# Kernel optimization log

Measured on AMD Instinct MI355X. Metric: run time of the kernel, lower is better.

The kernel has to match this reference:

```python
import jax, jax.numpy as jnp
import numpy as np

B, S, D = 2, 2048, 1024
H, DK = 16, 64
NUM_BUCKETS, MAX_DIST = 32, 128
EPS = 1e-6


def _relative_position_bucket(q_len, k_len):
    # T5 bidirectional relative position bucketing.
    ctx = jnp.arange(q_len)[:, None]
    mem = jnp.arange(k_len)[None, :]
    rel = mem - ctx  # [q, k]
    nb = NUM_BUCKETS // 2
    ret = (rel > 0).astype(jnp.int32) * nb
    n = jnp.abs(rel)
    max_exact = nb // 2
    is_small = n < max_exact
    n_safe = jnp.maximum(n, 1).astype(jnp.float32)
    val_large = max_exact + (
        jnp.log(n_safe / max_exact) / np.log(MAX_DIST / max_exact) * (nb - max_exact)
    ).astype(jnp.int32)
    val_large = jnp.minimum(val_large, nb - 1)
    return ret + jnp.where(is_small, n, val_large)  # [q, k] int32


def setup_inputs() -> dict:
    key = jax.random.key(0)
    ks = jax.random.split(key, 7)
    s = 0.02
    return {
        "hidden_states": jax.random.normal(ks[0], (B, S, D), jnp.float32),
        "ln_g": jnp.ones((D,), jnp.float32),
        "ln_b": jnp.zeros((D,), jnp.float32),
        "Wq": jax.random.normal(ks[1], (D, H * DK), jnp.float32) * s,
        "Wk": jax.random.normal(ks[2], (D, H * DK), jnp.float32) * s,
        "Wv": jax.random.normal(ks[3], (D, H * DK), jnp.float32) * s,
        "Wo": jax.random.normal(ks[4], (H * DK, D), jnp.float32) * s,
        "rel_bias": jax.random.normal(ks[5], (NUM_BUCKETS, H), jnp.float32) * s,
    }


def reference(hidden_states, ln_g, ln_b, Wq, Wk, Wv, Wo, rel_bias):
    b, s, d = hidden_states.shape
    # LayerNorm (nn.LayerNorm with affine, biased variance)
    mu = jnp.mean(hidden_states, axis=-1, keepdims=True)
    var = jnp.mean(jnp.square(hidden_states - mu), axis=-1, keepdims=True)
    normed = (hidden_states - mu) * jax.lax.rsqrt(var + EPS) * ln_g + ln_b
    # QKV projections (no bias), split heads
    q = (normed @ Wq).reshape(b, s, H, DK)
    k = (normed @ Wk).reshape(b, s, H, DK)
    v = (normed @ Wv).reshape(b, s, H, DK)
    # T5 attention: NO 1/sqrt(d) scaling; learned relative-position bias added to logits
    scores = jnp.einsum("bqhd,bkhd->bhqk", q, k)
    bucket = _relative_position_bucket(s, s)          # [s, s]
    bias = jnp.transpose(rel_bias[bucket], (2, 0, 1))  # [H, s, s]
    attn = jax.nn.softmax(scores + bias[None], axis=-1)
    ctx = jnp.einsum("bhqk,bkhd->bqhd", attn, v).reshape(b, s, H * DK)
    out = ctx @ Wo
    # residual (dropout is identity in eval)
    return hidden_states + out
```

## Files before the change

kernel.cpp:

```cpp
#include <hip/hip_runtime.h>
#include <hip/hip_bf16.h>
#include <math.h>

typedef __attribute__((__ext_vector_type__(8))) short bf16x8;
typedef __attribute__((__ext_vector_type__(4))) float f32x4;
typedef __attribute__((__ext_vector_type__(16))) float f32x16;
typedef __attribute__((__ext_vector_type__(4))) unsigned int u32x4;

#define B_ 2
#define S_ 2048
#define D_ 1024
#define H_ 16
#define DK_ 64
#define M_ (B_*S_)
#define N3_ 3072
#define BIAS_LEN 4096
#define M0_ 24.0f
#define L2E_ 1.4426950408889634f

__device__ __forceinline__ unsigned short f2bf(float f){
  union { float f; unsigned int u; } v; v.f = f;
  unsigned int u = v.u;
  unsigned int r = (u + 0x7fffu + ((u >> 16) & 1u)) >> 16;
  return (unsigned short)r;
}

__device__ __forceinline__ unsigned int pkbf(float a, float b){
  return ((unsigned int)f2bf(b) << 16) | (unsigned int)f2bf(a);
}

__device__ __forceinline__ float fexp2(float x){
#if __has_builtin(__builtin_amdgcn_exp2f)
  return __builtin_amdgcn_exp2f(x);
#else
  return __expf(x * 0.6931471805599453f);
#endif
}

__device__ __forceinline__ f32x4 zero4(){
  f32x4 z; z[0]=0.f; z[1]=0.f; z[2]=0.f; z[3]=0.f; return z;
}

__device__ __forceinline__ f32x4 mfma16(bf16x8 a, bf16x8 b, f32x4 c){
  return __builtin_amdgcn_mfma_f32_16x16x32_bf16(a, b, c, 0, 0, 0);
}
__device__ __forceinline__ f32x16 mfma32(bf16x8 a, bf16x8 b, f32x16 c){
  return __builtin_amdgcn_mfma_f32_32x32x16_bf16(a, b, c, 0, 0, 0);
}

__global__ __launch_bounds__(256) void transpose_cast_kernel(
    const float* __restrict__ Wq, const float* __restrict__ Wk,
    const float* __restrict__ Wv, const float* __restrict__ Wo,
    unsigned short* __restrict__ Wcat_t, unsigned short* __restrict__ Wo_t)
{
  __shared__ float tile[64][65];
  const int k0 = blockIdx.x * 64;
  const int v0 = blockIdx.y * 64;
  const int sel = v0 >> 10;
  const float* W = (sel==0) ? Wq : (sel==1) ? Wk : (sel==2) ? Wv : Wo;
  const int nn0 = v0 & 1023;
  #pragma unroll
  for (int i=0;i<16;i++){
    int idx = i*256 + threadIdx.x;
    int r = idx >> 6, c = idx & 63;
    tile[r][c] = W[(size_t)(k0+r)*1024 + nn0 + c];
  }
  __syncthreads();
  #pragma unroll
  for (int i=0;i<16;i++){
    int idx = i*256 + threadIdx.x;
    int nr = idx >> 6, kc = idx & 63;
    unsigned short bv = f2bf(tile[kc][nr]);
    if (sel < 3) Wcat_t[(size_t)(v0+nr)*1024 + k0 + kc] = bv;
    else         Wo_t[(size_t)(v0-3072+nr)*1024 + k0 + kc] = bv;
  }
}

__global__ __launch_bounds__(256) void bias_tab_kernel(
    const float* __restrict__ rel_bias, float* __restrict__ biasTab)
{
  int t = blockIdx.x*256 + threadIdx.x;
  if (t >= H_*BIAS_LEN) return;
  int h = t / BIAS_LEN;
  int idx = t - h*BIAS_LEN;
  int rel = idx - (S_-1);
  int ret = (rel > 0) ? 16 : 0;
  int n = (rel < 0) ? -rel : rel;
  int bidx;
  if (n < 8) bidx = n;
  else {
    float vl = logf((float)n * 0.125f) / 2.7725887f * 8.0f;
    int v = 8 + (int)vl;
    bidx = (v < 15) ? v : 15;
  }
  biasTab[t] = (rel_bias[(ret + bidx)*H_ + h] - M0_) * L2E_;
}

__global__ __launch_bounds__(256) void ln_kernel(
    const float* __restrict__ x, const float* __restrict__ g,
    const float* __restrict__ bta, unsigned short* __restrict__ out)
{
  const int row = blockIdx.x;
  const int tid = threadIdx.x;
  float4 v = ((const float4*)(x + (size_t)row*D_))[tid];
  float s  = v.x+v.y+v.z+v.w;
  float ss = v.x*v.x+v.y*v.y+v.z*v.z+v.w*v.w;
  #pragma unroll
  for (int off=1; off<64; off<<=1){ s += __shfl_xor(s,off,64); ss += __shfl_xor(ss,off,64); }
  __shared__ float rs[4], rss[4];
  const int wid = tid >> 6, lane = tid & 63;
  if (lane == 0){ rs[wid] = s; rss[wid] = ss; }
  __syncthreads();
  s  = rs[0]+rs[1]+rs[2]+rs[3];
  ss = rss[0]+rss[1]+rss[2]+rss[3];
  float mu  = s * (1.0f/1024.0f);
  float var = ss * (1.0f/1024.0f) - mu*mu;
  float rstd = rsqrtf(var + 1e-6f);
  float4 gg = ((const float4*)g)[tid];
  float4 bb = ((const float4*)bta)[tid];
  ushort4 o;
  o.x = f2bf((v.x-mu)*rstd*gg.x + bb.x);
  o.y = f2bf((v.y-mu)*rstd*gg.y + bb.y);
  o.z = f2bf((v.z-mu)*rstd*gg.z + bb.z);
  o.w = f2bf((v.w-mu)*rstd*gg.w + bb.w);
  ((ushort4*)(out + (size_t)row*D_))[tid] = o;
}

template<int MODE>
__global__ __launch_bounds__(256) void gemm_kernel(
    const unsigned short* __restrict__ A,
    const unsigned short* __restrict__ Bt,
    const float* __restrict__ resid,
    unsigned short* __restrict__ Qb,
    unsigned short* __restrict__ Kb,
    unsigned short* __restrict__ Vtb,
    float* __restrict__ outf,
    int Ndim, int Kdim)
{
  __shared__ unsigned short As[128][64];
  __shared__ unsigned short Bs[128][64];
  const int tid = threadIdx.x;
  const int wid = tid >> 6, lane = tid & 63;
  const int lr = lane & 15, lg = lane >> 4;
  const int wm = (wid >> 1) * 64, wn = (wid & 1) * 64;
  const int m0 = blockIdx.x * 128, n0 = blockIdx.y * 128;

  f32x4 acc[4][4];
  #pragma unroll
  for (int i=0;i<4;i++)
    #pragma unroll
    for (int j=0;j<4;j++) acc[i][j] = zero4();

  for (int k0 = 0; k0 < Kdim; k0 += 64) {
    __syncthreads();
    #pragma unroll
    for (int i=0;i<4;i++){
      int c = i*256 + tid;
      int row = c >> 3, ch = c & 7;
      bf16x8 av = *(const bf16x8*)(A  + (size_t)(m0+row)*Kdim + k0 + ch*8);
      *(bf16x8*)&As[row][(ch ^ (row & 7)) * 8] = av;
      bf16x8 bv = *(const bf16x8*)(Bt + (size_t)(n0+row)*Kdim + k0 + ch*8);
      *(bf16x8*)&Bs[row][(ch ^ (row & 7)) * 8] = bv;
    }
    __syncthreads();
    #pragma unroll
    for (int kk=0;kk<2;kk++){
      bf16x8 aF[4], bF[4];
      #pragma unroll
      for (int mi=0;mi<4;mi++){
        int row = wm + mi*16 + lr;
        aF[mi] = *(const bf16x8*)&As[row][((kk*4+lg) ^ (row & 7)) * 8];
      }
      #pragma unroll
      for (int ni=0;ni<4;ni++){
        int row = wn + ni*16 + lr;
        bF[ni] = *(const bf16x8*)&Bs[row][((kk*4+lg) ^ (row & 7)) * 8];
      }
      #pragma unroll
      for (int mi=0;mi<4;mi++)
        #pragma unroll
        for (int ni=0;ni<4;ni++)
          acc[mi][ni] = mfma16(aF[mi], bF[ni], acc[mi][ni]);
    }
  }

  #pragma unroll
  for (int mi=0;mi<4;mi++){
    #pragma unroll
    for (int ni=0;ni<4;ni++){
      #pragma unroll
      for (int r=0;r<4;r++){
        int m = m0 + wm + mi*16 + lg*4 + r;
        int n = n0 + wn + ni*16 + lr;
        float v = acc[mi][ni][r];
        if (MODE == 1) {
          outf[(size_t)m*Ndim + n] = v + resid[(size_t)m*Ndim + n];
        } else {
          int sel = n >> 10, nn = n & 1023;
          int h = nn >> 6, dk = nn & 63;
          int b = m >> 11, s = m & 2047;
          unsigned short bvv = f2bf(v);
          if (sel == 0)      Qb[(((size_t)(b*H_+h))*S_ + s)*DK_ + dk] = bvv;
          else if (sel == 1) Kb[(((size_t)(b*H_+h))*S_ + s)*DK_ + dk] = bvv;
          else               Vtb[(((size_t)(b*H_+h))*DK_ + dk)*S_ + s] = bvv;
        }
      }
    }
  }
}

__global__ __launch_bounds__(256, 2) void attn_kernel(
    const unsigned short* __restrict__ Qb,
    const unsigned short* __restrict__ Kb,
    const unsigned short* __restrict__ Vtb,
    const float* __restrict__ biasTab,
    const float* __restrict__ rel_bias,
    unsigned short* __restrict__ ctxb)
{
  __shared__ unsigned short Ks[64*64];
  __shared__ unsigned short Vts[64*64];
  __shared__ float biasW[2176];
  __shared__ float lshare[4][32];

  const int tid = threadIdx.x;
  const int wid = tid >> 6, lane = tid & 63;
  const int ql = lane & 31;
  const int hi = lane >> 5;
  const int bh = blockIdx.y;
  const int h = bh & (H_-1);
  const int b = bh >> 4;
  const int q0blk = blockIdx.x * 128;
  const int q0w = q0blk + wid*32;
  const int qlocal = wid*32 + ql;

  const int wb = 1920 - q0blk;
  for (int i = tid; i < 2176; i += 256) biasW[i] = biasTab[(size_t)h*BIAS_LEN + wb + i];

  const float cpos = (rel_bias[31*H_ + h] - M0_) * L2E_;
  const float cneg = (rel_bias[15*H_ + h] - M0_) * L2E_;

  const unsigned short* Qp = Qb + ((size_t)bh*S_ + q0w + ql)*DK_;
  bf16x8 qf[4];
  #pragma unroll
  for (int c=0;c<4;c++) qf[c] = *(const bf16x8*)(Qp + 16*c + 8*hi);

  const unsigned short* Ksrc = Kb  + (size_t)bh*S_*DK_;
  const unsigned short* Vsrc = Vtb + (size_t)bh*DK_*S_;
  const int c0 = tid, c1 = tid + 256;
  const int r0 = c0 >> 3, ch0 = c0 & 7;
  const int r1 = c1 >> 3, ch1 = c1 & 7;

  f32x16 acc[2];
  #pragma unroll
  for (int i=0;i<16;i++){ acc[0][i]=0.f; acc[1][i]=0.f; }
  float lsum = 0.f;

  bf16x8 sk0 = *(const bf16x8*)(Ksrc + (size_t)(0 + r0)*DK_ + ch0*8);
  bf16x8 sk1 = *(const bf16x8*)(Ksrc + (size_t)(0 + r1)*DK_ + ch1*8);
  bf16x8 sv0 = *(const bf16x8*)(Vsrc + (size_t)r0*S_ + 0 + ch0*8);
  bf16x8 sv1 = *(const bf16x8*)(Vsrc + (size_t)r1*S_ + 0 + ch1*8);

  for (int k0 = 0; k0 < S_; k0 += 64) {
    __syncthreads();
    *(bf16x8*)&Ks [r0*64 + ((ch0 ^ (r0&7))*8)] = sk0;
    *(bf16x8*)&Ks [r1*64 + ((ch1 ^ (r1&7))*8)] = sk1;
    *(bf16x8*)&Vts[r0*64 + ((ch0 ^ (r0&7))*8)] = sv0;
    *(bf16x8*)&Vts[r1*64 + ((ch1 ^ (r1&7))*8)] = sv1;
    __syncthreads();
    if (k0 + 64 < S_) {
      int kn = k0 + 64;
      sk0 = *(const bf16x8*)(Ksrc + (size_t)(kn + r0)*DK_ + ch0*8);
      sk1 = *(const bf16x8*)(Ksrc + (size_t)(kn + r1)*DK_ + ch1*8);
      sv0 = *(const bf16x8*)(Vsrc + (size_t)r0*S_ + kn + ch0*8);
      sv1 = *(const bf16x8*)(Vsrc + (size_t)r1*S_ + kn + ch1*8);
    }

    const bool uni_pos = (k0 >= q0w + 122);
    const bool uni_neg = (k0 + 63 <= q0w - 91);

    unsigned int W0[2][4], W1[2][4], O0[2][4], O1[2][4];

    #pragma unroll
    for (int st=0; st<2; ++st){
      f32x16 s;
      #pragma unroll
      for (int i=0;i<16;i++) s[i]=0.f;
      const int arow = st*32 + ql;
      #pragma unroll
      for (int c=0;c<4;c++){
        bf16x8 kf = *(const bf16x8*)&Ks[arow*64 + (((hi + 2*c) ^ (arow&7))*8)];
        s = mfma32(kf, qf[c], s);
      }
      float p[16];
      if (uni_pos) {
        #pragma unroll
        for (int r=0;r<16;r++) p[r] = fexp2(__builtin_fmaf(s[r], L2E_, cpos));
      } else if (uni_neg) {
        #pragma unroll
        for (int r=0;r<16;r++) p[r] = fexp2(__builtin_fmaf(s[r], L2E_, cneg));
      } else {
        #pragma unroll
        for (int r=0;r<16;r++){
          int key = k0 + st*32 + (r&3) + 8*(r>>2) + 4*hi;
          p[r] = fexp2(__builtin_fmaf(s[r], L2E_, biasW[key - qlocal + 127]));
        }
      }
      #pragma unroll
      for (int r=0;r<16;r++) lsum += p[r];
      #pragma unroll
      for (int m=0;m<4;m++){
        W0[st][m] = pkbf(p[4*m+0], p[4*m+1]);
        W1[st][m] = pkbf(p[4*m+2], p[4*m+3]);
        O0[st][m] = __shfl_xor(W0[st][m], 32);
        O1[st][m] = __shfl_xor(W1[st][m], 32);
      }
    }

    #pragma unroll
    for (int st=0; st<2; ++st){
      #pragma unroll
      for (int c=0;c<2;c++){
        unsigned int a0 = hi ? O0[st][2*c+1] : W0[st][2*c+0];
        unsigned int a1 = hi ? O1[st][2*c+1] : W1[st][2*c+0];
        unsigned int a2 = hi ? W0[st][2*c+1] : O0[st][2*c+0];
        unsigned int a3 = hi ? W1[st][2*c+1] : O1[st][2*c+0];
        u32x4 pu; pu[0]=a0; pu[1]=a1; pu[2]=a2; pu[3]=a3;
        bf16x8 pav = __builtin_bit_cast(bf16x8, pu);
        const int vch = 4*st + 2*c + hi;
        #pragma unroll
        for (int dt=0; dt<2; ++dt){
          const int vrow = ql + 32*dt;
          bf16x8 vf = *(const bf16x8*)&Vts[vrow*64 + ((vch ^ (vrow&7))*8)];
          acc[dt] = mfma32(pav, vf, acc[dt]);
        }
      }
    }
  }

  float ltot = lsum + __shfl_xor(lsum, 32);
  lshare[wid][ql] = 1.0f / ltot;
  __syncthreads();
  #pragma unroll
  for (int r=0;r<16;r++){
    const int qr = (r&3) + 8*(r>>2) + 4*hi;
    const float li = lshare[wid][qr];
    const int q = q0w + qr;
    #pragma unroll
    for (int dt=0; dt<2; ++dt){
      const int d = ql + 32*dt;
      ctxb[((size_t)(b*S_ + q))*(H_*DK_) + h*DK_ + d] = f2bf(acc[dt][r] * li);
    }
  }
}

extern "C" void kernel_launch(void* const* d_in, const int* in_sizes, int n_in,
                              void* d_out, int out_size, void* d_ws, size_t ws_size,
                              hipStream_t stream) {
  const float* hidden   = (const float*)d_in[0];
  const float* ln_g     = (const float*)d_in[1];
  const float* ln_b     = (const float*)d_in[2];
  const float* Wq       = (const float*)d_in[3];
  const float* Wk       = (const float*)d_in[4];
  const float* Wv       = (const float*)d_in[5];
  const float* Wo       = (const float*)d_in[6];
  const float* rel_bias = (const float*)d_in[7];
  float* out = (float*)d_out;

  char* ws = (char*)d_ws;
  const size_t off_ln   = 0;
  const size_t off_wcat = 8388608;
  const size_t off_wo   = 14680064;
  const size_t off_q    = 16777216;
  const size_t off_k    = 25165824;
  const size_t off_vt   = 33554432;
  const size_t off_ctx  = 41943040;
  const size_t off_bias = 50331648;

  unsigned short* ln_out  = (unsigned short*)(ws + off_ln);
  unsigned short* Wcat_t  = (unsigned short*)(ws + off_wcat);
  unsigned short* Wo_t    = (unsigned short*)(ws + off_wo);
  unsigned short* Qb      = (unsigned short*)(ws + off_q);
  unsigned short* Kb      = (unsigned short*)(ws + off_k);
  unsigned short* Vtb     = (unsigned short*)(ws + off_vt);
  unsigned short* ctxb    = (unsigned short*)(ws + off_ctx);
  float*          biasTab = (float*)(ws + off_bias);

  transpose_cast_kernel<<<dim3(16,64), 256, 0, stream>>>(Wq, Wk, Wv, Wo, Wcat_t, Wo_t);
  bias_tab_kernel<<<(H_*BIAS_LEN + 255)/256, 256, 0, stream>>>(rel_bias, biasTab);
  ln_kernel<<<M_, 256, 0, stream>>>(hidden, ln_g, ln_b, ln_out);
  gemm_kernel<0><<<dim3(M_/128, N3_/128), 256, 0, stream>>>(
      ln_out, Wcat_t, nullptr, Qb, Kb, Vtb, nullptr, N3_, D_);
  attn_kernel<<<dim3(S_/128, B_*H_), 256, 0, stream>>>(Qb, Kb, Vtb, biasTab, rel_bias, ctxb);
  gemm_kernel<1><<<dim3(M_/128, D_/128), 256, 0, stream>>>(
      ctxb, Wo_t, hidden, nullptr, nullptr, nullptr, out, D_, D_);
}
```

Baseline: 137.9 us.

## Use hardware bf16 pack, direct global-to-LDS loads, tile swizzle, vectorized V stores

Replaces software bf16 rounding with the v_cvt_pk_bf16_f32 instruction in layernorm, the GEMM epilogue and the attention probabilities. The GEMM now stages A/B tiles with global_load_lds, applying the XOR swizzle on the global side, and remaps block indices so nearby tiles share cache. The QKV epilogue specializes per Q/K/V tile, and V-transposed stores become packed 8-byte writes. The aim is to cut VALU conversion cost, register staging and scattered stores, but the hardware conversion may round special values differently and the tile remap assumes the grid size divides by 8.

```diff
diff --git a/kernel.cpp b/kernel.cpp
--- a/kernel.cpp
+++ b/kernel.cpp
@@ -18,15 +18,15 @@
 #define M0_ 24.0f
 #define L2E_ 1.4426950408889634f
 
+__device__ __forceinline__ unsigned int cvtpk(float a, float b){
+  unsigned int r;
+  asm("v_cvt_pk_bf16_f32 %0, %1, %2" : "=v"(r) : "v"(a), "v"(b));
+  return r;
+}
 __device__ __forceinline__ unsigned short f2bf(float f){
-  union { float f; unsigned int u; } v; v.f = f;
-  unsigned int u = v.u;
-  unsigned int r = (u + 0x7fffu + ((u >> 16) & 1u)) >> 16;
+  unsigned int r;
+  asm("v_cvt_pk_bf16_f32 %0, %1, %2" : "=v"(r) : "v"(f), "v"(f));
   return (unsigned short)r;
-}
-
-__device__ __forceinline__ unsigned int pkbf(float a, float b){
-  return ((unsigned int)f2bf(b) << 16) | (unsigned int)f2bf(a);
 }
 
 __device__ __forceinline__ float fexp2(float x){
@@ -46,6 +46,12 @@
 }
 __device__ __forceinline__ f32x16 mfma32(bf16x8 a, bf16x8 b, f32x16 c){
   return __builtin_amdgcn_mfma_f32_32x32x16_bf16(a, b, c, 0, 0, 0);
+}
+
+__device__ __forceinline__ void gload16(const void* g, void* l){
+  __builtin_amdgcn_global_load_lds(
+      (const __attribute__((address_space(1))) void*)g,
+      (__attribute__((address_space(3))) void*)l, 16, 0, 0);
 }
 
 __global__ __launch_bounds__(256) void transpose_cast_kernel(
@@ -118,12 +124,10 @@
   float rstd = rsqrtf(var + 1e-6f);
   float4 gg = ((const float4*)g)[tid];
   float4 bb = ((const float4*)bta)[tid];
-  ushort4 o;
-  o.x = f2bf((v.x-mu)*rstd*gg.x + bb.x);
-  o.y = f2bf((v.y-mu)*rstd*gg.y + bb.y);
-  o.z = f2bf((v.z-mu)*rstd*gg.z + bb.z);
-  o.w = f2bf((v.w-mu)*rstd*gg.w + bb.w);
-  ((ushort4*)(out + (size_t)row*D_))[tid] = o;
+  uint2 o;
+  o.x = cvtpk((v.x-mu)*rstd*gg.x + bb.x, (v.y-mu)*rstd*gg.y + bb.y);
+  o.y = cvtpk((v.z-mu)*rstd*gg.z + bb.z, (v.w-mu)*rstd*gg.w + bb.w);
+  ((uint2*)(out + (size_t)row*D_))[tid] = o;
 }
 
 template<int MODE>
@@ -137,13 +141,18 @@
     float* __restrict__ outf,
     int Ndim, int Kdim)
 {
-  __shared__ unsigned short As[128][64];
-  __shared__ unsigned short Bs[128][64];
+  __shared__ unsigned short As[128*64];
+  __shared__ unsigned short Bs[128*64];
   const int tid = threadIdx.x;
   const int wid = tid >> 6, lane = tid & 63;
   const int lr = lane & 15, lg = lane >> 4;
   const int wm = (wid >> 1) * 64, wn = (wid & 1) * 64;
-  const int m0 = blockIdx.x * 128, n0 = blockIdx.y * 128;
+
+  const int nbx = gridDim.x;
+  const int total = nbx * gridDim.y;
+  const int flat = blockIdx.y * nbx + blockIdx.x;
+  const int swz = (flat & 7) * (total >> 3) + (flat >> 3);
+  const int m0 = (swz % nbx) * 128, n0 = (swz / nbx) * 128;
 
   f32x4 acc[4][4];
   #pragma unroll
@@ -157,10 +166,9 @@
     for (int i=0;i<4;i++){
       int c = i*256 + tid;
       int row = c >> 3, ch = c & 7;
-      bf16x8 av = *(const bf16x8*)(A  + (size_t)(m0+row)*Kdim + k0 + ch*8);
-      *(bf16x8*)&As[row][(ch ^ (row & 7)) * 8] = av;
-      bf16x8 bv = *(const bf16x8*)(Bt + (size_t)(n0+row)*Kdim + k0 + ch*8);
-      *(bf16x8*)&Bs[row][(ch ^ (row & 7)) * 8] = bv;
+      int chs = ch ^ (row & 7);
+      gload16(A  + (size_t)(m0+row)*Kdim + k0 + chs*8, As + c*8);
+      gload16(Bt + (size_t)(n0+row)*Kdim + k0 + chs*8, Bs + c*8);
     }
     __syncthreads();
     #pragma unroll
@@ -169,12 +177,12 @@
       #pragma unroll
       for (int mi=0;mi<4;mi++){
         int row = wm + mi*16 + lr;
-        aF[mi] = *(const bf16x8*)&As[row][((kk*4+lg) ^ (row & 7)) * 8];
+        aF[mi] = *(const bf16x8*)&As[row*64 + (((kk*4+lg) ^ (row & 7)) * 8)];
       }
       #pragma unroll
       for (int ni=0;ni<4;ni++){
         int row = wn + ni*16 + lr;
-        bF[ni] = *(const bf16x8*)&Bs[row][((kk*4+lg) ^ (row & 7)) * 8];
+        bF[ni] = *(const bf16x8*)&Bs[row*64 + (((kk*4+lg) ^ (row & 7)) * 8)];
       }
       #pragma unroll
       for (int mi=0;mi<4;mi++)
@@ -184,27 +192,47 @@
     }
   }
 
-  #pragma unroll
-  for (int mi=0;mi<4;mi++){
-    #pragma unroll
-    for (int ni=0;ni<4;ni++){
-      #pragma unroll
-      for (int r=0;r<4;r++){
-        int m = m0 + wm + mi*16 + lg*4 + r;
-        int n = n0 + wn + ni*16 + lr;
-        float v = acc[mi][ni][r];
-        if (MODE == 1) {
-          outf[(size_t)m*Ndim + n] = v + resid[(size_t)m*Ndim + n];
-        } else {
-          int sel = n >> 10, nn = n & 1023;
-          int h = nn >> 6, dk = nn & 63;
+  if (MODE == 1) {
+    #pragma unroll
+    for (int mi=0;mi<4;mi++)
+      #pragma unroll
+      for (int ni=0;ni<4;ni++)
+        #pragma unroll
+        for (int r=0;r<4;r++){
+          int m = m0 + wm + mi*16 + lg*4 + r;
+          int n = n0 + wn + ni*16 + lr;
+          outf[(size_t)m*Ndim + n] = acc[mi][ni][r] + resid[(size_t)m*Ndim + n];
+        }
+  } else {
+    const int seln = n0 >> 10;
+    if (seln == 2) {
+      #pragma unroll
+      for (int mi=0;mi<4;mi++)
+        #pragma unroll
+        for (int ni=0;ni<4;ni++){
+          int m = m0 + wm + mi*16 + lg*4;
+          int n = n0 + wn + ni*16 + lr;
+          int nn = n & 1023, hh = nn >> 6, dk = nn & 63;
           int b = m >> 11, s = m & 2047;
-          unsigned short bvv = f2bf(v);
-          if (sel == 0)      Qb[(((size_t)(b*H_+h))*S_ + s)*DK_ + dk] = bvv;
-          else if (sel == 1) Kb[(((size_t)(b*H_+h))*S_ + s)*DK_ + dk] = bvv;
-          else               Vtb[(((size_t)(b*H_+h))*DK_ + dk)*S_ + s] = bvv;
+          uint2 u;
+          u.x = cvtpk(acc[mi][ni][0], acc[mi][ni][1]);
+          u.y = cvtpk(acc[mi][ni][2], acc[mi][ni][3]);
+          *(uint2*)(Vtb + (((size_t)(b*H_+hh))*DK_ + dk)*S_ + s) = u;
         }
-      }
+    } else {
+      unsigned short* __restrict__ dst = (seln == 0) ? Qb : Kb;
+      #pragma unroll
+      for (int mi=0;mi<4;mi++)
+        #pragma unroll
+        for (int ni=0;ni<4;ni++)
+          #pragma unroll
+          for (int r=0;r<4;r++){
+            int m = m0 + wm + mi*16 + lg*4 + r;
+            int n = n0 + wn + ni*16 + lr;
+            int nn = n & 1023, hh = nn >> 6, dk = nn & 63;
+            int b = m >> 11, s = m & 2047;
+            dst[(((size_t)(b*H_+hh))*S_ + s)*DK_ + dk] = f2bf(acc[mi][ni][r]);
+          }
     }
   }
 }
@@ -309,8 +337,8 @@
       for (int r=0;r<16;r++) lsum += p[r];
       #pragma unroll
       for (int m=0;m<4;m++){
-        W0[st][m] = pkbf(p[4*m+0], p[4*m+1]);
-        W1[st][m] = pkbf(p[4*m+2], p[4*m+3]);
+        W0[st][m] = cvtpk(p[4*m+0], p[4*m+1]);
+        W1[st][m] = cvtpk(p[4*m+2], p[4*m+3]);
         O0[st][m] = __shfl_xor(W0[st][m], 32);
         O1[st][m] = __shfl_xor(W1[st][m], 32);
       }
```

Result: no change. 139.5 us (+1.1%).
